# Optimization experiments

Measured on AMD Instinct MI355X. Metric: run time of the kernel, lower is better.

The kernel has to match this reference:

```python
import jax, jax.numpy as jnp
import numpy as np

B, T, E, H = 8, 2048, 256, 8
D = E // H  # head_size = 32
EPS = 1e-5  # torch LayerNorm default


def _layernorm(x, g, b):
    m = jnp.mean(x, axis=-1, keepdims=True)
    v = jnp.var(x, axis=-1, keepdims=True)
    return (x - m) / jnp.sqrt(v + EPS) * g + b


def setup_inputs() -> dict:
    key = jax.random.key(0)
    ks = jax.random.split(key, 9)
    s = lambda k, shape, fan: (jax.random.normal(k, shape, jnp.float32) / np.sqrt(fan)).astype(jnp.float32)
    return {
        "x": jax.random.normal(ks[0], (B, T, E), jnp.float32),
        "wq": s(ks[1], (H, E, D), E),
        "wk": s(ks[2], (H, E, D), E),
        "wv": s(ks[3], (H, E, D), E),
        "w_lin": s(ks[4], (E, E), E),
        "b_lin": jnp.zeros((E,), jnp.float32),
        "g1": jnp.ones((E,), jnp.float32),
        "beta1": jnp.zeros((E,), jnp.float32),
        "g2": jnp.ones((E,), jnp.float32),
        "beta2": jnp.zeros((E,), jnp.float32),
        "w_f1": s(ks[5], (E, 4 * E), E),
        "b_f1": jnp.zeros((4 * E,), jnp.float32),
        "w_f2": s(ks[6], (4 * E, E), 4 * E),
        "b_f2": jnp.zeros((E,), jnp.float32),
    }


def reference(x, wq, wk, wv, w_lin, b_lin, g1, beta1, g2, beta2, w_f1, b_f1, w_f2, b_f2):
    b, t, e = x.shape
    xn = _layernorm(x, g1, beta1)  # norm1
    # all heads at once: (B,T,E) x (H,E,D) -> (B,H,T,D)
    q = jnp.einsum('bte,hed->bhtd', xn, wq)
    k = jnp.einsum('bte,hed->bhtd', xn, wk)
    v = jnp.einsum('bte,hed->bhtd', xn, wv)
    # scale uses C = embedding_size (as in source, not head_size)
    scores = jnp.einsum('bhtd,bhsd->bhts', q, k) * (e ** -0.5)
    mask = jnp.tril(jnp.ones((t, t), bool))  # (query t, key s)
    scores = jnp.where(mask[None, None, :, :], scores, -jnp.inf)
    # source applies softmax over dim=1 of (B,T,T) = the QUERY axis -> axis 2 of bhts
    attn = jax.nn.softmax(scores, axis=2)
    heads = jnp.einsum('bhts,bhsd->bhtd', attn, v)
    heads = heads.transpose(0, 2, 1, 3).reshape(b, t, e)  # concat over heads
    xh = xn + heads  # residual around attention
    xl = xh @ w_lin + b_lin  # projection (dropout is identity at eval)
    x2 = _layernorm(xl, g2, beta2)  # norm2
    ff = jax.nn.relu(x2 @ w_f1 + b_f1) @ w_f2 + b_f2  # FFN (dropout identity)
    return x2 + ff
```

## Files before the change

### kernel.cpp

```cpp
#include <hip/hip_runtime.h>
#include <math.h>

#define TT 2048
#define TE 256
#define NTOK 16384
#define QSCALE (0.0625f * 1.44269504088896f)

typedef short  bf16x8 __attribute__((ext_vector_type(8)));
typedef float  f32x4  __attribute__((ext_vector_type(4)));
typedef float  f32x16 __attribute__((ext_vector_type(16)));
typedef unsigned short u16x4 __attribute__((ext_vector_type(4)));
typedef unsigned short u16x8 __attribute__((ext_vector_type(8)));

__device__ __forceinline__ unsigned short f2b(float f) {
    union { float f; unsigned int u; } v; v.f = f;
    unsigned int r = v.u + 0x7FFF + ((v.u >> 16) & 1);
    return (unsigned short)(r >> 16);
}
__device__ __forceinline__ float b2f(unsigned short u) {
    union { unsigned int i; float f; } v; v.i = ((unsigned int)u) << 16;
    return v.f;
}
#if __has_builtin(__builtin_amdgcn_cvt_pk_bf16_f32)
__device__ __forceinline__ unsigned int pk_bf16(float a, float b) {
    typedef __bf16 bf2 __attribute__((ext_vector_type(2)));
    union { bf2 v; unsigned int u; } u;
    u.v = __builtin_amdgcn_cvt_pk_bf16_f32(a, b);
    return u.u;
}
#else
__device__ __forceinline__ unsigned int pk_bf16(float a, float b) {
    return (unsigned int)f2b(a) | ((unsigned int)f2b(b) << 16);
}
#endif
#if __has_builtin(__builtin_amdgcn_exp2f)
#define FEXP2(x) __builtin_amdgcn_exp2f(x)
#else
#define FEXP2(x) __expf(0.69314718056f * (x))
#endif
__device__ __forceinline__ void pswap(unsigned &a, unsigned &b) {
#if __has_builtin(__builtin_amdgcn_permlane32_swap)
    auto r = __builtin_amdgcn_permlane32_swap(a, b, false, false);
    a = r[0]; b = r[1];
#else
    asm("v_permlane32_swap_b32 %0, %1" : "+v"(a), "+v"(b));
#endif
}
__device__ __forceinline__ bf16x8 ld8(const unsigned short* p) {
    return *(const bf16x8*)p;
}
__device__ __forceinline__ void gl_lds16(const unsigned short* g, unsigned short* l) {
    __builtin_amdgcn_global_load_lds(
        (const __attribute__((address_space(1))) unsigned int*)(uintptr_t)g,
        (__attribute__((address_space(3))) unsigned int*)(uintptr_t)l,
        16, 0, 0);
}
#define MFMA16(a, b, c) __builtin_amdgcn_mfma_f32_16x16x32_bf16((a), (b), (c), 0, 0, 0)
#define MFMA32(a, b, c) __builtin_amdgcn_mfma_f32_32x32x16_bf16((a), (b), (c), 0, 0, 0)
#define SETPRIO(n) __builtin_amdgcn_s_setprio(n)


__device__ __forceinline__ void soft_pv(const f32x16 st, bf16x8 vv0, bf16x8 vv1,
                                        bool diag, int hi, int l31, f32x16& acc) {
    unsigned Wd[8];
    if (diag) {
#pragma unroll
        for (int j = 0; j < 8; ++j) {
            int r0 = 2 * j;
            int s0 = (r0 & 3) + 8 * (r0 >> 2) + 4 * hi;
            float e0 = (s0 <= l31)     ? FEXP2(st[r0])     : 0.f;
            float e1 = (s0 + 1 <= l31) ? FEXP2(st[r0 + 1]) : 0.f;
            Wd[j] = pk_bf16(e0, e1);
        }
    } else {
#pragma unroll
        for (int j = 0; j < 8; ++j)
            Wd[j] = pk_bf16(FEXP2(st[2 * j]), FEXP2(st[2 * j + 1]));
    }
    pswap(Wd[0], Wd[2]); pswap(Wd[1], Wd[3]);
    pswap(Wd[4], Wd[6]); pswap(Wd[5], Wd[7]);
    union { unsigned u4[4]; bf16x8 v; } pa0, pa1;
    pa0.u4[0] = Wd[0]; pa0.u4[1] = Wd[1]; pa0.u4[2] = Wd[2]; pa0.u4[3] = Wd[3];
    pa1.u4[0] = Wd[4]; pa1.u4[1] = Wd[5]; pa1.u4[2] = Wd[6]; pa1.u4[3] = Wd[7];
    SETPRIO(1);
    acc = MFMA32(pa0.v, vv0, acc);
    acc = MFMA32(pa1.v, vv1, acc);
    SETPRIO(0);
}

__device__ __forceinline__ void accum_exp(const f32x16 st, bool diag,
                                          int hi, int l31, float* acc) {
    if (diag) {
#pragma unroll
        for (int r = 0; r < 16; ++r) {
            int s_local = (r & 3) + 8 * (r >> 2) + 4 * hi;
            acc[r] += (l31 >= s_local) ? FEXP2(st[r]) : 0.f;
        }
    } else {
#pragma unroll
        for (int r = 0; r < 16; ++r) acc[r] += FEXP2(st[r]);
    }
}

__global__ __launch_bounds__(256) void prep(const float* __restrict__ wq,
                                            const float* __restrict__ wk,
                                            const float* __restrict__ wv,
                                            const float* __restrict__ w_lin,
                                            const float* __restrict__ w_f1,
                                            const float* __restrict__ w_f2,
                                            unsigned short* __restrict__ Wqkv,
                                            unsigned short* __restrict__ Wlin,
                                            unsigned short* __restrict__ Wf1,
                                            unsigned short* __restrict__ Wf2,
                                            const float* __restrict__ X,
                                            const float* __restrict__ g,
                                            const float* __restrict__ bta,
                                            unsigned short* __restrict__ Yb) {
    if (blockIdx.x >= 3072) {
        int row = (blockIdx.x - 3072) * 4 + (threadIdx.x >> 6);
        int lane = threadIdx.x & 63;
        const float4 v = *(const float4*)&X[(size_t)row * TE + lane * 4];
        float s = v.x + v.y + v.z + v.w;
        float s2 = v.x * v.x + v.y * v.y + v.z * v.z + v.w * v.w;
#pragma unroll
        for (int off = 1; off <= 32; off <<= 1) {
            s  += __shfl_xor(s,  off, 64);
            s2 += __shfl_xor(s2, off, 64);
        }
        float mean = s * (1.0f / TE);
        float var = s2 * (1.0f / TE) - mean * mean;
        float rstd = rsqrtf(var + 1e-5f);
        const float4 gg = *(const float4*)&g[lane * 4];
        const float4 bb = *(const float4*)&bta[lane * 4];
        u16x4 ob = { f2b((v.x - mean) * rstd * gg.x + bb.x),
                     f2b((v.y - mean) * rstd * gg.y + bb.y),
                     f2b((v.z - mean) * rstd * gg.z + bb.z),
                     f2b((v.w - mean) * rstd * gg.w + bb.w) };
        *(u16x4*)&Yb[(size_t)row * TE + lane * 4] = ob;
        return;
    }
    int idx = blockIdx.x * 256 + threadIdx.x;
    if (idx < 196608) {
        int n = idx >> 8, k = idx & 255;
        int which = n >> 8, h = (n >> 5) & 7, d = n & 31;
        const float* w = (which == 0) ? wq : (which == 1) ? wk : wv;
        Wqkv[idx] = f2b(w[(h * 256 + k) * 32 + d]);
    } else if (idx < 262144) {
        int i = idx - 196608; int n = i >> 8, k = i & 255;
        Wlin[i] = f2b(w_lin[k * 256 + n]);
    } else if (idx < 524288) {
        int i = idx - 262144; int n = i >> 8, k = i & 255;
        Wf1[i] = f2b(w_f1[k * 1024 + n]);
    } else {
        int i = idx - 524288; int n = i >> 10, k = i & 1023;
        Wf2[i] = f2b(w_f2[k * 256 + n]);
    }
}

__global__ __launch_bounds__(256) void ln2_red(const float* __restrict__ Pp,
                                               const float* __restrict__ bias,
                                               const float* __restrict__ g,
                                               const float* __restrict__ bta,
                                               unsigned short* __restrict__ Yb) {
    int row = blockIdx.x * 4 + (threadIdx.x >> 6);
    int lane = threadIdx.x & 63;
    size_t base = (size_t)row * TE + lane * 4;
    const float4 p0 = *(const float4*)&Pp[base];
    const float4 bl = *(const float4*)&bias[lane * 4];
    float4 v;
    v.x = p0.x + bl.x; v.y = p0.y + bl.y;
    v.z = p0.z + bl.z; v.w = p0.w + bl.w;
    float s = v.x + v.y + v.z + v.w;
    float s2 = v.x * v.x + v.y * v.y + v.z * v.z + v.w * v.w;
#pragma unroll
    for (int off = 1; off <= 32; off <<= 1) {
        s  += __shfl_xor(s,  off, 64);
        s2 += __shfl_xor(s2, off, 64);
    }
    float mean = s * (1.0f / TE);
    float var = s2 * (1.0f / TE) - mean * mean;
    float rstd = rsqrtf(var + 1e-5f);
    const float4 gg = *(const float4*)&g[lane * 4];
    const float4 bb = *(const float4*)&bta[lane * 4];
    u16x4 ob = { f2b((v.x - mean) * rstd * gg.x + bb.x),
                 f2b((v.y - mean) * rstd * gg.y + bb.y),
                 f2b((v.z - mean) * rstd * gg.z + bb.z),
                 f2b((v.w - mean) * rstd * gg.w + bb.w) };
    *(u16x4*)&Yb[base] = ob;
}

template<int KS>
__global__ __launch_bounds__(256) void gemm_lds(const unsigned short* __restrict__ A,
                                                int lda,
                                                const unsigned short* __restrict__ Bt,
                                                int ldb,
                                                const float* __restrict__ bias,
                                                const unsigned short* __restrict__ resid,
                                                float* __restrict__ outF,
                                                unsigned short* __restrict__ outB,
                                                int N, int relu) {
    __shared__ unsigned short LDSb[3 * 2048 + 3 * 4096];
    unsigned short* Al = LDSb;
    unsigned short* Bl = LDSb + 3 * 2048;
    int tid = threadIdx.x;
    int w = tid >> 6, lane = tid & 63, q = lane >> 4, col = lane & 15;
    int wm = w & 1, wn = w >> 1;
    int m0 = blockIdx.x * 64;
    int n0 = blockIdx.y * 128;
    f32x4 acc[2][4] = {};
    int srow = lane >> 2;
    int skq  = ((lane & 3) ^ ((srow >> 1) & 3)) * 8;
    const unsigned short* Ag0 = A  + (size_t)(m0 + w * 16 + srow) * lda + skq;
    const unsigned short* Bg0 = Bt + (size_t)(n0 + w * 32 + srow) * ldb + skq;
    const unsigned short* Bg1 = Bg0 + (size_t)16 * ldb;
    int rq = (q ^ ((col >> 1) & 3)) * 8;
#define G_STAGE(bf, kk) do { \
        gl_lds16(Ag0 + (kk), &Al[(bf) * 2048 + (w * 16) * 32]); \
        gl_lds16(Bg0 + (kk), &Bl[(bf) * 4096 + (w * 32) * 32]); \
        gl_lds16(Bg1 + (kk), &Bl[(bf) * 4096 + (w * 32 + 16) * 32]); \
    } while (0)
    G_STAGE(0, 0);
    G_STAGE(1, 32);
#pragma unroll
    for (int k0 = 0; k0 < KS; k0 += 32) {
        const int jb = (k0 >> 5) % 3;
        if (k0 + 32 < KS) { asm volatile("s_waitcnt vmcnt(3)" ::: "memory"); }
        else              { asm volatile("s_waitcnt vmcnt(0)" ::: "memory"); }
        __builtin_amdgcn_s_barrier();
        if (k0 + 64 < KS) G_STAGE((jb + 2) % 3, k0 + 64);
        bf16x8 a[2], b[4];
#pragma unroll
        for (int i = 0; i < 2; ++i)
            a[i] = ld8(&Al[jb * 2048 + (wm * 32 + i * 16 + col) * 32 + rq]);
#pragma unroll
        for (int j = 0; j < 4; ++j)
            b[j] = ld8(&Bl[jb * 4096 + (wn * 64 + j * 16 + col) * 32 + rq]);
#pragma unroll
        for (int i = 0; i < 2; ++i)
#pragma unroll
            for (int j = 0; j < 4; ++j)
                acc[i][j] = MFMA16(a[i], b[j], acc[i][j]);
        __builtin_amdgcn_sched_barrier(0);
    }
#undef G_STAGE
    float* Cb = (float*)LDSb;
    const int CLD = 132;
#pragma unroll
    for (int i = 0; i < 2; ++i) {
        __syncthreads();
#pragma unroll
        for (int j = 0; j < 4; ++j)
#pragma unroll
            for (int r = 0; r < 4; ++r)
                Cb[(wm * 16 + q * 4 + r) * CLD + wn * 64 + j * 16 + col] = acc[i][j][r];
        __syncthreads();
        int row = tid >> 3;
        int seg = (tid & 7) * 16;
        int mloc = (row & 15) + i * 16 + (row >> 4) * 32;
        int m = m0 + mloc;
        int n = n0 + seg;
        float vbuf[16];
#pragma unroll
        for (int u = 0; u < 16; ++u) vbuf[u] = Cb[row * CLD + seg + u];
        if (bias) {
#pragma unroll
            for (int u4 = 0; u4 < 4; ++u4) {
                float4 bb = *(const float4*)&bias[n + u4 * 4];
                vbuf[u4 * 4 + 0] += bb.x; vbuf[u4 * 4 + 1] += bb.y;
                vbuf[u4 * 4 + 2] += bb.z; vbuf[u4 * 4 + 3] += bb.w;
            }
        }
        if (resid) {
            u16x8 r0 = *(const u16x8*)&resid[(size_t)m * N + n];
            u16x8 r1 = *(const u16x8*)&resid[(size_t)m * N + n + 8];
#pragma unroll
            for (int u = 0; u < 8; ++u) {
                vbuf[u]     += b2f(r0[u]);
                vbuf[8 + u] += b2f(r1[u]);
            }
        }
        if (relu) {
#pragma unroll
            for (int u = 0; u < 16; ++u) vbuf[u] = fmaxf(vbuf[u], 0.f);
        }
        if (outF) {
#pragma unroll
            for (int u = 0; u < 16; u += 4)
                *(float4*)&outF[(size_t)m * N + n + u] = *(const float4*)&vbuf[u];
        }
        if (outB) {
            u16x8 o0, o1;
#pragma unroll
            for (int u = 0; u < 8; ++u) { o0[u] = f2b(vbuf[u]); o1[u] = f2b(vbuf[8 + u]); }
            *(u16x8*)&outB[(size_t)m * N + n] = o0;
            *(u16x8*)&outB[(size_t)m * N + n + 8] = o1;
        }
    }
}

__global__ __launch_bounds__(256) void gemm_qkv(const unsigned short* __restrict__ A,
                                                const unsigned short* __restrict__ Bt,
                                                unsigned short* __restrict__ Qd,
                                                unsigned short* __restrict__ Kd,
                                                unsigned short* __restrict__ Vc) {
    const int K = 256;
    __shared__ unsigned short LDSb[3 * 2048 + 3 * 4096];
    unsigned short* Al = LDSb;
    unsigned short* Bl = LDSb + 3 * 2048;
    int tid = threadIdx.x;
    int w = tid >> 6, lane = tid & 63, q = lane >> 4, col = lane & 15;
    int wm = w & 1, wn = w >> 1;
    int m0 = blockIdx.x * 64;
    int n0 = blockIdx.y * 128;
    f32x4 acc[2][4] = {};
    int srow = lane >> 2;
    int skq  = ((lane & 3) ^ ((srow >> 1) & 3)) * 8;
    const unsigned short* Ag0 = A  + (size_t)(m0 + w * 16 + srow) * K + skq;
    const unsigned short* Bg0 = Bt + (size_t)(n0 + w * 32 + srow) * K + skq;
    const unsigned short* Bg1 = Bg0 + (size_t)16 * K;
    int rq = (q ^ ((col >> 1) & 3)) * 8;
#define G_STAGE(bf, kk) do { \
        gl_lds16(Ag0 + (kk), &Al[(bf) * 2048 + (w * 16) * 32]); \
        gl_lds16(Bg0 + (kk), &Bl[(bf) * 4096 + (w * 32) * 32]); \
        gl_lds16(Bg1 + (kk), &Bl[(bf) * 4096 + (w * 32 + 16) * 32]); \
    } while (0)
    G_STAGE(0, 0);
    G_STAGE(1, 32);
#pragma unroll
    for (int k0 = 0; k0 < K; k0 += 32) {
        const int jb = (k0 >> 5) % 3;
        if (k0 + 32 < K) { asm volatile("s_waitcnt vmcnt(3)" ::: "memory"); }
        else             { asm volatile("s_waitcnt vmcnt(0)" ::: "memory"); }
        __builtin_amdgcn_s_barrier();
        if (k0 + 64 < K) G_STAGE((jb + 2) % 3, k0 + 64);
        bf16x8 a[2], b[4];
#pragma unroll
        for (int i = 0; i < 2; ++i)
            a[i] = ld8(&Al[jb * 2048 + (wm * 32 + i * 16 + col) * 32 + rq]);
#pragma unroll
        for (int j = 0; j < 4; ++j)
            b[j] = ld8(&Bl[jb * 4096 + (wn * 64 + j * 16 + col) * 32 + rq]);
#pragma unroll
        for (int i = 0; i < 2; ++i)
#pragma unroll
            for (int j = 0; j < 4; ++j)
                acc[i][j] = MFMA16(a[i], b[j], acc[i][j]);
        __builtin_amdgcn_sched_barrier(0);
    }
#undef G_STAGE
#pragma unroll
    for (int i = 0; i < 2; ++i)
#pragma unroll
    for (int j = 0; j < 4; ++j) {
        int n = n0 + wn * 64 + j * 16 + col;
        int which = n >> 8, h = (n >> 5) & 7, d = n & 31;
        int m = m0 + wm * 32 + i * 16 + q * 4;
        int b = m >> 11, t = m & 2047;
        int bh = b * 8 + h;
        if (which == 0) {
            size_t qb = ((size_t)(bh * 2 + (d >> 4)) * TT + t) * 16 + (d & 15);
#pragma unroll
            for (int r = 0; r < 4; ++r)
                Qd[qb + r * 16] = f2b(acc[i][j][r] * QSCALE);
        } else if (which == 1) {
            size_t kb = ((size_t)(bh * 2 + (d >> 4)) * TT + t) * 16 + (d & 15);
#pragma unroll
            for (int r = 0; r < 4; ++r)
                Kd[kb + r * 16] = f2b(acc[i][j][r]);
        } else {
            uint2 pv;
            pv.x = pk_bf16(acc[i][j][0], acc[i][j][1]);
            pv.y = pk_bf16(acc[i][j][2], acc[i][j][3]);
            *(uint2*)&Vc[(((size_t)bh * 256 + (t >> 3)) * 32 + d) * 8 + (t & 7)] = pv;
        }
    }
}

__global__ __launch_bounds__(256, 2) void attn_cols(const unsigned short* __restrict__ Qd,
                                                    const unsigned short* __restrict__ Kd,
                                                    unsigned short* __restrict__ Vc) {
    __shared__ float Lb[4][32];
    __shared__ float Linv[32];
    int tid = threadIdx.x;
    int w = tid >> 6, lane = tid & 63, hi = lane >> 5, l31 = lane & 31;
    int bh = blockIdx.x;
    int u = blockIdx.y;
    const unsigned short* Qb = Qd + ((size_t)bh * 2 * TT + l31) * 16 + hi * 8;
    const unsigned short* Kb = Kd + ((size_t)bh * 2 * TT + l31) * 16 + hi * 8;
    const f32x16 z16 = {};
#pragma unroll
    for (int phase = 0; phase < 2; ++phase) {
        int stile = phase ? (63 - u) : u;
        int sbase = stile * 32;
        bf16x8 a0 = ld8(Kb + (size_t)sbase * 16);
        bf16x8 a1 = ld8(Kb + ((size_t)TT + sbase) * 16);
        float acc[16] = {};
        int c = stile + w;
        bool diagP = (w == 0);
        bf16x8 qP0, qP1, qQ0, qQ1;
        if (c < 64) {
            qP0 = ld8(Qb + (size_t)(c * 32) * 16);
            qP1 = ld8(Qb + ((size_t)TT + c * 32) * 16);
        }
        if (c + 4 < 64) {
            qQ0 = ld8(Qb + (size_t)((c + 4) * 32) * 16);
            qQ1 = ld8(Qb + ((size_t)TT + (c + 4) * 32) * 16);
        }
        while (c + 8 < 64) {
            SETPRIO(1);
            f32x16 stP = MFMA32(a0, qP0, z16); stP = MFMA32(a1, qP1, stP);
            SETPRIO(0);
            qP0 = ld8(Qb + (size_t)((c + 8) * 32) * 16);
            qP1 = ld8(Qb + ((size_t)TT + (c + 8) * 32) * 16);
            SETPRIO(1);
            f32x16 stQ = MFMA32(a0, qQ0, z16); stQ = MFMA32(a1, qQ1, stQ);
            SETPRIO(0);
            accum_exp(stP, diagP, hi, l31, acc); diagP = false;
            if (c + 12 < 64) {
                qQ0 = ld8(Qb + (size_t)((c + 12) * 32) * 16);
                qQ1 = ld8(Qb + ((size_t)TT + (c + 12) * 32) * 16);
            }
            accum_exp(stQ, false, hi, l31, acc);
            c += 8;
        }
        if (c < 64) {
            f32x16 stP = MFMA32(a0, qP0, z16); stP = MFMA32(a1, qP1, stP);
            accum_exp(stP, diagP, hi, l31, acc);
        }
        if (c + 4 < 64) {
            f32x16 stQ = MFMA32(a0, qQ0, z16); stQ = MFMA32(a1, qQ1, stQ);
            accum_exp(stQ, false, hi, l31, acc);
        }
#pragma unroll
        for (int off = 1; off <= 16; off <<= 1)
#pragma unroll
            for (int r = 0; r < 16; ++r) acc[r] += __shfl_xor(acc[r], off, 64);
        if (l31 == 0) {
#pragma unroll
            for (int r = 0; r < 16; ++r) {
                int s_local = (r & 3) + 8 * (r >> 2) + 4 * hi;
                Lb[w][s_local] = acc[r];
            }
        }
        __syncthreads();
        if (tid < 32)
            Linv[tid] = 1.0f / (Lb[0][tid] + Lb[1][tid] + Lb[2][tid] + Lb[3][tid]);
        __syncthreads();
        if (tid < 128) {
            int sbl = tid >> 5;
            int d = tid & 31;
            size_t base = (((size_t)bh * 256 + stile * 4 + sbl) * 32 + d) * 8;
            u16x8 v = *(const u16x8*)&Vc[base];
            u16x8 o;
#pragma unroll
            for (int e = 0; e < 8; ++e) o[e] = f2b(b2f(v[e]) * Linv[sbl * 8 + e]);
            *(u16x8*)&Vc[base] = o;
        }
        __syncthreads();
    }
}

__global__ __launch_bounds__(256, 2) void attn_out(const unsigned short* __restrict__ Qd,
                                                   const unsigned short* __restrict__ Kd,
                                                   const unsigned short* __restrict__ Vc,
                                                   const unsigned short* __restrict__ xnb,
                                                   unsigned short* __restrict__ xh_bf) {
    __shared__ float Ob[4][16][36];
    int tid = threadIdx.x;
    int w = tid >> 6, lane = tid & 63, hi = lane >> 5, l31 = lane & 31;
    int bh = blockIdx.x, b = bh >> 3, h = bh & 7;
    int u = blockIdx.y;
    const unsigned short* Kb = Kd + ((size_t)bh * 2 * TT + l31) * 16 + hi * 8;
    const unsigned short* Vb = Vc + (size_t)bh * 65536 + hi * 256 + l31 * 8;
    const unsigned short* Qbase = Qd + ((size_t)bh * 2 * TT + l31) * 16 + hi * 8;
    const f32x16 z16 = {};

#pragma unroll
    for (int phase = 0; phase < 2; ++phase) {
        int tt = phase ? (63 - u) : u;
        int tbase = tt * 32;
        bf16x8 q0 = ld8(Qbase + (size_t)tbase * 16);
        bf16x8 q1 = ld8(Qbase + ((size_t)TT + tbase) * 16);
        f32x16 acc = z16;

        int c = w;
        bf16x8 kP0, kP1, vP0, vP1, kQ0, kQ1, vQ0, vQ1;
        if (c <= tt) {
            kP0 = ld8(Kb + (size_t)c * 512);
            kP1 = ld8(Kb + (size_t)TT * 16 + (size_t)c * 512);
            vP0 = ld8(Vb + (size_t)c * 1024);
            vP1 = ld8(Vb + (size_t)c * 1024 + 512);
        }
        if (c + 4 <= tt) {
            kQ0 = ld8(Kb + (size_t)(c + 4) * 512);
            kQ1 = ld8(Kb + (size_t)TT * 16 + (size_t)(c + 4) * 512);
            vQ0 = ld8(Vb + (size_t)(c + 4) * 1024);
            vQ1 = ld8(Vb + (size_t)(c + 4) * 1024 + 512);
        }
        while (c + 8 <= tt) {
            SETPRIO(1);
            f32x16 stP = MFMA32(kP0, q0, z16); stP = MFMA32(kP1, q1, stP);
            SETPRIO(0);
            kP0 = ld8(Kb + (size_t)(c + 8) * 512);
            kP1 = ld8(Kb + (size_t)TT * 16 + (size_t)(c + 8) * 512);
            SETPRIO(1);
            f32x16 stQ = MFMA32(kQ0, q0, z16); stQ = MFMA32(kQ1, q1, stQ);
            SETPRIO(0);
            soft_pv(stP, vP0, vP1, false, hi, l31, acc);
            vP0 = ld8(Vb + (size_t)(c + 8) * 1024);
            vP1 = ld8(Vb + (size_t)(c + 8) * 1024 + 512);
            if (c + 12 <= tt) {
                kQ0 = ld8(Kb + (size_t)(c + 12) * 512);
                kQ1 = ld8(Kb + (size_t)TT * 16 + (size_t)(c + 12) * 512);
            }
            soft_pv(stQ, vQ0, vQ1, false, hi, l31, acc);
            if (c + 12 <= tt) {
                vQ0 = ld8(Vb + (size_t)(c + 12) * 1024);
                vQ1 = ld8(Vb + (size_t)(c + 12) * 1024 + 512);
            }
            c += 8;
        }
        if (c <= tt) {
            f32x16 stP = MFMA32(kP0, q0, z16); stP = MFMA32(kP1, q1, stP);
            soft_pv(stP, vP0, vP1, c == tt, hi, l31, acc);
        }
        if (c + 4 <= tt) {
            f32x16 stQ = MFMA32(kQ0, q0, z16); stQ = MFMA32(kQ1, q1, stQ);
            soft_pv(stQ, vQ0, vQ1, c + 4 == tt, hi, l31, acc);
        }

#pragma unroll
        for (int half = 0; half < 2; ++half) {
#pragma unroll
            for (int rr = 0; rr < 8; ++rr) {
                int r = half * 8 + rr;
                int t16 = (r & 3) + 8 * ((r >> 2) & 1) + 4 * hi;
                Ob[w][t16][l31] = acc[r];
            }
            __syncthreads();
            if (tid < 128) {
                int row = tid >> 3;
                int c4 = (tid & 7) * 4;
                float4 s0 = *(const float4*)&Ob[0][row][c4];
                float4 s1 = *(const float4*)&Ob[1][row][c4];
                float4 s2 = *(const float4*)&Ob[2][row][c4];
                float4 s3 = *(const float4*)&Ob[3][row][c4];
                size_t base = ((size_t)(b * TT) + tbase + half * 16 + row) * TE
                              + h * 32 + c4;
                u16x4 xv = *(const u16x4*)&xnb[base];
                u16x4 ob = { f2b(s0.x + s1.x + s2.x + s3.x + b2f(xv[0])),
                             f2b(s0.y + s1.y + s2.y + s3.y + b2f(xv[1])),
                             f2b(s0.z + s1.z + s2.z + s3.z + b2f(xv[2])),
                             f2b(s0.w + s1.w + s2.w + s3.w + b2f(xv[3])) };
                *(u16x4*)&xh_bf[base] = ob;
            }
            __syncthreads();
        }
    }
}

extern "C" void kernel_launch(void* const* d_in, const int* in_sizes, int n_in,
                              void* d_out, int out_size, void* d_ws, size_t ws_size,
                              hipStream_t stream) {
    (void)in_sizes; (void)n_in; (void)out_size; (void)ws_size;
    const float* x     = (const float*)d_in[0];
    const float* wq    = (const float*)d_in[1];
    const float* wk    = (const float*)d_in[2];
    const float* wv    = (const float*)d_in[3];
    const float* w_lin = (const float*)d_in[4];
    const float* b_lin = (const float*)d_in[5];
    const float* g1    = (const float*)d_in[6];
    const float* beta1 = (const float*)d_in[7];
    const float* g2    = (const float*)d_in[8];
    const float* beta2 = (const float*)d_in[9];
    const float* w_f1  = (const float*)d_in[10];
    const float* b_f1  = (const float*)d_in[11];
    const float* w_f2  = (const float*)d_in[12];
    const float* b_f2  = (const float*)d_in[13];
    float* out = (float*)d_out;

    char* ws = (char*)d_ws;
    unsigned short* Wqkv_t = (unsigned short*)(ws + 0);
    unsigned short* Wlin_t = (unsigned short*)(ws + 393216);
    unsigned short* Wf1_t  = (unsigned short*)(ws + 524288);
    unsigned short* Wf2_t  = (unsigned short*)(ws + 1048576);
    unsigned short* xn_bf  = (unsigned short*)(ws + 2097152);
    unsigned short* Qbf    = (unsigned short*)(ws + 10485760);
    unsigned short* Kbf    = (unsigned short*)(ws + 18874368);
    unsigned short* Vt     = (unsigned short*)(ws + 27262976);
    unsigned short* xh_bf  = (unsigned short*)(ws + 35651584);
    float*          Pp     = (float*)(ws + 44040192);
    unsigned short* x2_bf  = xn_bf;
    unsigned short* h_bf   = Qbf;

    prep<<<7168, 256, 0, stream>>>(wq, wk, wv, w_lin, w_f1, w_f2,
                                   Wqkv_t, Wlin_t, Wf1_t, Wf2_t,
                                   x, g1, beta1, xn_bf);
    gemm_qkv<<<dim3(256, 6), 256, 0, stream>>>(xn_bf, Wqkv_t, Qbf, Kbf, Vt);
    attn_cols<<<dim3(64, 32), 256, 0, stream>>>(Qbf, Kbf, Vt);
    attn_out<<<dim3(64, 32), 256, 0, stream>>>(Qbf, Kbf, Vt, xn_bf, xh_bf);
    gemm_lds<256><<<dim3(256, 2), 256, 0, stream>>>(xh_bf, 256, Wlin_t, 256,
                                                    nullptr, nullptr, Pp, nullptr, 256, 0);
    ln2_red<<<4096, 256, 0, stream>>>(Pp, b_lin, g2, beta2, x2_bf);
    gemm_lds<256><<<dim3(256, 8), 256, 0, stream>>>(x2_bf, 256, Wf1_t, 256,
                                                    b_f1, nullptr, nullptr, h_bf, 1024, 1);
    gemm_lds<1024><<<dim3(256, 2), 256, 0, stream>>>(h_bf, 1024, Wf2_t, 1024,
                                                     b_f2, x2_bf, out, nullptr, 256, 0);
}
```

Baseline: 225.8 us.

## Tile weight transposes through LDS and split attention blocks to one tile each

The weight-prep path now transposes weights with 64x64 tiles staged in shared memory, so global reads and writes are coalesced. Before, each thread did one strided scalar gather, and the prep grid shrinks accordingly. Both attention kernels drop the paired-tile (u, 63-u) load-balancing loop and launch one block per tile, doubling the grid. This raises parallelism but makes per-block work uneven under the causal mask.

```diff
diff --git a/kernel.cpp b/kernel.cpp
--- a/kernel.cpp
+++ b/kernel.cpp
@@ -116,8 +116,9 @@
                                             const float* __restrict__ g,
                                             const float* __restrict__ bta,
                                             unsigned short* __restrict__ Yb) {
-    if (blockIdx.x >= 3072) {
-        int row = (blockIdx.x - 3072) * 4 + (threadIdx.x >> 6);
+    int bid = blockIdx.x;
+    if (bid >= 240) {
+        int row = (bid - 240) * 4 + (threadIdx.x >> 6);
         int lane = threadIdx.x & 63;
         const float4 v = *(const float4*)&X[(size_t)row * TE + lane * 4];
         float s = v.x + v.y + v.z + v.w;
@@ -139,21 +140,43 @@
         *(u16x4*)&Yb[(size_t)row * TE + lane * 4] = ob;
         return;
     }
-    int idx = blockIdx.x * 256 + threadIdx.x;
-    if (idx < 196608) {
-        int n = idx >> 8, k = idx & 255;
-        int which = n >> 8, h = (n >> 5) & 7, d = n & 31;
-        const float* w = (which == 0) ? wq : (which == 1) ? wk : wv;
-        Wqkv[idx] = f2b(w[(h * 256 + k) * 32 + d]);
-    } else if (idx < 262144) {
-        int i = idx - 196608; int n = i >> 8, k = i & 255;
-        Wlin[i] = f2b(w_lin[k * 256 + n]);
-    } else if (idx < 524288) {
-        int i = idx - 262144; int n = i >> 8, k = i & 255;
-        Wf1[i] = f2b(w_f1[k * 1024 + n]);
-    } else {
-        int i = idx - 524288; int n = i >> 10, k = i & 1023;
-        Wf2[i] = f2b(w_f2[k * 256 + n]);
+    __shared__ unsigned short Tt[64][65];
+    int t = threadIdx.x;
+    if (bid < 96) {
+        int which = bid / 32, h = (bid >> 2) & 7, kt = bid & 3;
+        const float* src = ((which == 0) ? wq : (which == 1) ? wk : wv)
+                           + (size_t)h * 256 * 32;
+        int d = t & 31, kr = t >> 5;
+#pragma unroll
+        for (int r = 0; r < 8; ++r) {
+            int kl = kr * 8 + r;
+            Tt[kl][d] = f2b(src[(size_t)(kt * 64 + kl) * 32 + d]);
+        }
+        __syncthreads();
+        int kl = t & 63, dr = t >> 6;
+#pragma unroll
+        for (int r = 0; r < 8; ++r) {
+            int dl = dr * 8 + r;
+            Wqkv[(size_t)(which * 256 + h * 32 + dl) * 256 + kt * 64 + kl] = Tt[kl][dl];
+        }
+        return;
+    }
+    const float* src; unsigned short* dst; int ldn, ldk, kt, nt;
+    if (bid < 112)      { int b2 = bid - 96;  src = w_lin; dst = Wlin; ldn = 256;  ldk = 256;  kt = b2 & 3;  nt = b2 >> 2; }
+    else if (bid < 176) { int b3 = bid - 112; src = w_f1;  dst = Wf1;  ldn = 1024; ldk = 256;  kt = b3 >> 4; nt = b3 & 15; }
+    else                { int b4 = bid - 176; src = w_f2;  dst = Wf2;  ldn = 256;  ldk = 1024; kt = b4 >> 2; nt = b4 & 3; }
+    int n = t & 63, kr = t >> 6;
+#pragma unroll
+    for (int r = 0; r < 16; ++r) {
+        int kl = kr * 16 + r;
+        Tt[kl][n] = f2b(src[(size_t)(kt * 64 + kl) * ldn + nt * 64 + n]);
+    }
+    __syncthreads();
+    int klane = t & 63, nr = t >> 6;
+#pragma unroll
+    for (int r = 0; r < 16; ++r) {
+        int nl = nr * 16 + r;
+        dst[(size_t)(nt * 64 + nl) * ldk + kt * 64 + klane] = Tt[klane][nl];
     }
 }
 
@@ -384,79 +407,74 @@
     int tid = threadIdx.x;
     int w = tid >> 6, lane = tid & 63, hi = lane >> 5, l31 = lane & 31;
     int bh = blockIdx.x;
-    int u = blockIdx.y;
+    int stile = blockIdx.y;
     const unsigned short* Qb = Qd + ((size_t)bh * 2 * TT + l31) * 16 + hi * 8;
     const unsigned short* Kb = Kd + ((size_t)bh * 2 * TT + l31) * 16 + hi * 8;
     const f32x16 z16 = {};
-#pragma unroll
-    for (int phase = 0; phase < 2; ++phase) {
-        int stile = phase ? (63 - u) : u;
-        int sbase = stile * 32;
-        bf16x8 a0 = ld8(Kb + (size_t)sbase * 16);
-        bf16x8 a1 = ld8(Kb + ((size_t)TT + sbase) * 16);
-        float acc[16] = {};
-        int c = stile + w;
-        bool diagP = (w == 0);
-        bf16x8 qP0, qP1, qQ0, qQ1;
-        if (c < 64) {
-            qP0 = ld8(Qb + (size_t)(c * 32) * 16);
-            qP1 = ld8(Qb + ((size_t)TT + c * 32) * 16);
-        }
-        if (c + 4 < 64) {
-            qQ0 = ld8(Qb + (size_t)((c + 4) * 32) * 16);
-            qQ1 = ld8(Qb + ((size_t)TT + (c + 4) * 32) * 16);
-        }
-        while (c + 8 < 64) {
-            SETPRIO(1);
-            f32x16 stP = MFMA32(a0, qP0, z16); stP = MFMA32(a1, qP1, stP);
-            SETPRIO(0);
-            qP0 = ld8(Qb + (size_t)((c + 8) * 32) * 16);
-            qP1 = ld8(Qb + ((size_t)TT + (c + 8) * 32) * 16);
-            SETPRIO(1);
-            f32x16 stQ = MFMA32(a0, qQ0, z16); stQ = MFMA32(a1, qQ1, stQ);
-            SETPRIO(0);
-            accum_exp(stP, diagP, hi, l31, acc); diagP = false;
-            if (c + 12 < 64) {
-                qQ0 = ld8(Qb + (size_t)((c + 12) * 32) * 16);
-                qQ1 = ld8(Qb + ((size_t)TT + (c + 12) * 32) * 16);
-            }
-            accum_exp(stQ, false, hi, l31, acc);
-            c += 8;
-        }
-        if (c < 64) {
-            f32x16 stP = MFMA32(a0, qP0, z16); stP = MFMA32(a1, qP1, stP);
-            accum_exp(stP, diagP, hi, l31, acc);
-        }
-        if (c + 4 < 64) {
-            f32x16 stQ = MFMA32(a0, qQ0, z16); stQ = MFMA32(a1, qQ1, stQ);
-            accum_exp(stQ, false, hi, l31, acc);
-        }
-#pragma unroll
-        for (int off = 1; off <= 16; off <<= 1)
-#pragma unroll
-            for (int r = 0; r < 16; ++r) acc[r] += __shfl_xor(acc[r], off, 64);
-        if (l31 == 0) {
-#pragma unroll
-            for (int r = 0; r < 16; ++r) {
-                int s_local = (r & 3) + 8 * (r >> 2) + 4 * hi;
-                Lb[w][s_local] = acc[r];
-            }
-        }
-        __syncthreads();
-        if (tid < 32)
-            Linv[tid] = 1.0f / (Lb[0][tid] + Lb[1][tid] + Lb[2][tid] + Lb[3][tid]);
-        __syncthreads();
-        if (tid < 128) {
-            int sbl = tid >> 5;
-            int d = tid & 31;
-            size_t base = (((size_t)bh * 256 + stile * 4 + sbl) * 32 + d) * 8;
-            u16x8 v = *(const u16x8*)&Vc[base];
-            u16x8 o;
-#pragma unroll
-            for (int e = 0; e < 8; ++e) o[e] = f2b(b2f(v[e]) * Linv[sbl * 8 + e]);
-            *(u16x8*)&Vc[base] = o;
-        }
-        __syncthreads();
+    int sbase = stile * 32;
+    bf16x8 a0 = ld8(Kb + (size_t)sbase * 16);
+    bf16x8 a1 = ld8(Kb + ((size_t)TT + sbase) * 16);
+    float acc[16] = {};
+    int c = stile + w;
+    bool diagP = (w == 0);
+    bf16x8 qP0, qP1, qQ0, qQ1;
+    if (c < 64) {
+        qP0 = ld8(Qb + (size_t)(c * 32) * 16);
+        qP1 = ld8(Qb + ((size_t)TT + c * 32) * 16);
+    }
+    if (c + 4 < 64) {
+        qQ0 = ld8(Qb + (size_t)((c + 4) * 32) * 16);
+        qQ1 = ld8(Qb + ((size_t)TT + (c + 4) * 32) * 16);
+    }
+    while (c + 8 < 64) {
+        SETPRIO(1);
+        f32x16 stP = MFMA32(a0, qP0, z16); stP = MFMA32(a1, qP1, stP);
+        SETPRIO(0);
+        qP0 = ld8(Qb + (size_t)((c + 8) * 32) * 16);
+        qP1 = ld8(Qb + ((size_t)TT + (c + 8) * 32) * 16);
+        SETPRIO(1);
+        f32x16 stQ = MFMA32(a0, qQ0, z16); stQ = MFMA32(a1, qQ1, stQ);
+        SETPRIO(0);
+        accum_exp(stP, diagP, hi, l31, acc); diagP = false;
+        if (c + 12 < 64) {
+            qQ0 = ld8(Qb + (size_t)((c + 12) * 32) * 16);
+            qQ1 = ld8(Qb + ((size_t)TT + (c + 12) * 32) * 16);
+        }
+        accum_exp(stQ, false, hi, l31, acc);
+        c += 8;
+    }
+    if (c < 64) {
+        f32x16 stP = MFMA32(a0, qP0, z16); stP = MFMA32(a1, qP1, stP);
+        accum_exp(stP, diagP, hi, l31, acc);
+    }
+    if (c + 4 < 64) {
+        f32x16 stQ = MFMA32(a0, qQ0, z16); stQ = MFMA32(a1, qQ1, stQ);
+        accum_exp(stQ, false, hi, l31, acc);
+    }
+#pragma unroll
+    for (int off = 1; off <= 16; off <<= 1)
+#pragma unroll
+        for (int r = 0; r < 16; ++r) acc[r] += __shfl_xor(acc[r], off, 64);
+    if (l31 == 0) {
+#pragma unroll
+        for (int r = 0; r < 16; ++r) {
+            int s_local = (r & 3) + 8 * (r >> 2) + 4 * hi;
+            Lb[w][s_local] = acc[r];
+        }
+    }
+    __syncthreads();
+    if (tid < 32)
+        Linv[tid] = 1.0f / (Lb[0][tid] + Lb[1][tid] + Lb[2][tid] + Lb[3][tid]);
+    __syncthreads();
+    if (tid < 128) {
+        int sbl = tid >> 5;
+        int d = tid & 31;
+        size_t base = (((size_t)bh * 256 + stile * 4 + sbl) * 32 + d) * 8;
+        u16x8 v = *(const u16x8*)&Vc[base];
+        u16x8 o;
+#pragma unroll
+        for (int e = 0; e < 8; ++e) o[e] = f2b(b2f(v[e]) * Linv[sbl * 8 + e]);
+        *(u16x8*)&Vc[base] = o;
     }
 }
 
@@ -469,93 +487,89 @@
     int tid = threadIdx.x;
     int w = tid >> 6, lane = tid & 63, hi = lane >> 5, l31 = lane & 31;
     int bh = blockIdx.x, b = bh >> 3, h = bh & 7;
-    int u = blockIdx.y;
+    int tt = blockIdx.y;
     const unsigned short* Kb = Kd + ((size_t)bh * 2 * TT + l31) * 16 + hi * 8;
     const unsigned short* Vb = Vc + (size_t)bh * 65536 + hi * 256 + l31 * 8;
     const unsigned short* Qbase = Qd + ((size_t)bh * 2 * TT + l31) * 16 + hi * 8;
     const f32x16 z16 = {};
 
-#pragma unroll
-    for (int phase = 0; phase < 2; ++phase) {
-        int tt = phase ? (63 - u) : u;
-        int tbase = tt * 32;
-        bf16x8 q0 = ld8(Qbase + (size_t)tbase * 16);
-        bf16x8 q1 = ld8(Qbase + ((size_t)TT + tbase) * 16);
-        f32x16 acc = z16;
-
-        int c = w;
-        bf16x8 kP0, kP1, vP0, vP1, kQ0, kQ1, vQ0, vQ1;
-        if (c <= tt) {
-            kP0 = ld8(Kb + (size_t)c * 512);
-            kP1 = ld8(Kb + (size_t)TT * 16 + (size_t)c * 512);
-            vP0 = ld8(Vb + (size_t)c * 1024);
-            vP1 = ld8(Vb + (size_t)c * 1024 + 512);
-        }
-        if (c + 4 <= tt) {
-            kQ0 = ld8(Kb + (size_t)(c + 4) * 512);
-            kQ1 = ld8(Kb + (size_t)TT * 16 + (size_t)(c + 4) * 512);
-            vQ0 = ld8(Vb + (size_t)(c + 4) * 1024);
-            vQ1 = ld8(Vb + (size_t)(c + 4) * 1024 + 512);
-        }
-        while (c + 8 <= tt) {
-            SETPRIO(1);
-            f32x16 stP = MFMA32(kP0, q0, z16); stP = MFMA32(kP1, q1, stP);
-            SETPRIO(0);
-            kP0 = ld8(Kb + (size_t)(c + 8) * 512);
-            kP1 = ld8(Kb + (size_t)TT * 16 + (size_t)(c + 8) * 512);
-            SETPRIO(1);
-            f32x16 stQ = MFMA32(kQ0, q0, z16); stQ = MFMA32(kQ1, q1, stQ);
-            SETPRIO(0);
-            soft_pv(stP, vP0, vP1, false, hi, l31, acc);
-            vP0 = ld8(Vb + (size_t)(c + 8) * 1024);
-            vP1 = ld8(Vb + (size_t)(c + 8) * 1024 + 512);
-            if (c + 12 <= tt) {
-                kQ0 = ld8(Kb + (size_t)(c + 12) * 512);
-                kQ1 = ld8(Kb + (size_t)TT * 16 + (size_t)(c + 12) * 512);
-            }
-            soft_pv(stQ, vQ0, vQ1, false, hi, l31, acc);
-            if (c + 12 <= tt) {
-                vQ0 = ld8(Vb + (size_t)(c + 12) * 1024);
-                vQ1 = ld8(Vb + (size_t)(c + 12) * 1024 + 512);
-            }
-            c += 8;
-        }
-        if (c <= tt) {
-            f32x16 stP = MFMA32(kP0, q0, z16); stP = MFMA32(kP1, q1, stP);
-            soft_pv(stP, vP0, vP1, c == tt, hi, l31, acc);
-        }
-        if (c + 4 <= tt) {
-            f32x16 stQ = MFMA32(kQ0, q0, z16); stQ = MFMA32(kQ1, q1, stQ);
-            soft_pv(stQ, vQ0, vQ1, c + 4 == tt, hi, l31, acc);
-        }
-
-#pragma unroll
-        for (int half = 0; half < 2; ++half) {
-#pragma unroll
-            for (int rr = 0; rr < 8; ++rr) {
-                int r = half * 8 + rr;
-                int t16 = (r & 3) + 8 * ((r >> 2) & 1) + 4 * hi;
-                Ob[w][t16][l31] = acc[r];
-            }
-            __syncthreads();
-            if (tid < 128) {
-                int row = tid >> 3;
-                int c4 = (tid & 7) * 4;
-                float4 s0 = *(const float4*)&Ob[0][row][c4];
-                float4 s1 = *(const float4*)&Ob[1][row][c4];
-                float4 s2 = *(const float4*)&Ob[2][row][c4];
-                float4 s3 = *(const float4*)&Ob[3][row][c4];
-                size_t base = ((size_t)(b * TT) + tbase + half * 16 + row) * TE
-                              + h * 32 + c4;
-                u16x4 xv = *(const u16x4*)&xnb[base];
-                u16x4 ob = { f2b(s0.x + s1.x + s2.x + s3.x + b2f(xv[0])),
-                             f2b(s0.y + s1.y + s2.y + s3.y + b2f(xv[1])),
-                             f2b(s0.z + s1.z + s2.z + s3.z + b2f(xv[2])),
-                             f2b(s0.w + s1.w + s2.w + s3.w + b2f(xv[3])) };
-                *(u16x4*)&xh_bf[base] = ob;
-            }
-            __syncthreads();
-        }
+    int tbase = tt * 32;
+    bf16x8 q0 = ld8(Qbase + (size_t)tbase * 16);
+    bf16x8 q1 = ld8(Qbase + ((size_t)TT + tbase) * 16);
+    f32x16 acc = z16;
+
+    int c = w;
+    bf16x8 kP0, kP1, vP0, vP1, kQ0, kQ1, vQ0, vQ1;
+    if (c <= tt) {
+        kP0 = ld8(Kb + (size_t)c * 512);
+        kP1 = ld8(Kb + (size_t)TT * 16 + (size_t)c * 512);
+        vP0 = ld8(Vb + (size_t)c * 1024);
+        vP1 = ld8(Vb + (size_t)c * 1024 + 512);
+    }
+    if (c + 4 <= tt) {
+        kQ0 = ld8(Kb + (size_t)(c + 4) * 512);
+        kQ1 = ld8(Kb + (size_t)TT * 16 + (size_t)(c + 4) * 512);
+        vQ0 = ld8(Vb + (size_t)(c + 4) * 1024);
+        vQ1 = ld8(Vb + (size_t)(c + 4) * 1024 + 512);
+    }
+    while (c + 8 <= tt) {
+        SETPRIO(1);
+        f32x16 stP = MFMA32(kP0, q0, z16); stP = MFMA32(kP1, q1, stP);
+        SETPRIO(0);
+        kP0 = ld8(Kb + (size_t)(c + 8) * 512);
+        kP1 = ld8(Kb + (size_t)TT * 16 + (size_t)(c + 8) * 512);
+        SETPRIO(1);
+        f32x16 stQ = MFMA32(kQ0, q0, z16); stQ = MFMA32(kQ1, q1, stQ);
+        SETPRIO(0);
+        soft_pv(stP, vP0, vP1, false, hi, l31, acc);
+        vP0 = ld8(Vb + (size_t)(c + 8) * 1024);
+        vP1 = ld8(Vb + (size_t)(c + 8) * 1024 + 512);
+        if (c + 12 <= tt) {
+            kQ0 = ld8(Kb + (size_t)(c + 12) * 512);
+            kQ1 = ld8(Kb + (size_t)TT * 16 + (size_t)(c + 12) * 512);
+        }
+        soft_pv(stQ, vQ0, vQ1, false, hi, l31, acc);
+        if (c + 12 <= tt) {
+            vQ0 = ld8(Vb + (size_t)(c + 12) * 1024);
+            vQ1 = ld8(Vb + (size_t)(c + 12) * 1024 + 512);
+        }
+        c += 8;
+    }
+    if (c <= tt) {
+        f32x16 stP = MFMA32(kP0, q0, z16); stP = MFMA32(kP1, q1, stP);
+        soft_pv(stP, vP0, vP1, c == tt, hi, l31, acc);
+    }
+    if (c + 4 <= tt) {
+        f32x16 stQ = MFMA32(kQ0, q0, z16); stQ = MFMA32(kQ1, q1, stQ);
+        soft_pv(stQ, vQ0, vQ1, c + 4 == tt, hi, l31, acc);
+    }
+
+#pragma unroll
+    for (int half = 0; half < 2; ++half) {
+#pragma unroll
+        for (int rr = 0; rr < 8; ++rr) {
+            int r = half * 8 + rr;
+            int t16 = (r & 3) + 8 * ((r >> 2) & 1) + 4 * hi;
+            Ob[w][t16][l31] = acc[r];
+        }
+        __syncthreads();
+        if (tid < 128) {
+            int row = tid >> 3;
+            int c4 = (tid & 7) * 4;
+            float4 s0 = *(const float4*)&Ob[0][row][c4];
+            float4 s1 = *(const float4*)&Ob[1][row][c4];
+            float4 s2 = *(const float4*)&Ob[2][row][c4];
+            float4 s3 = *(const float4*)&Ob[3][row][c4];
+            size_t base = ((size_t)(b * TT) + tbase + half * 16 + row) * TE
+                          + h * 32 + c4;
+            u16x4 xv = *(const u16x4*)&xnb[base];
+            u16x4 ob = { f2b(s0.x + s1.x + s2.x + s3.x + b2f(xv[0])),
+                         f2b(s0.y + s1.y + s2.y + s3.y + b2f(xv[1])),
+                         f2b(s0.z + s1.z + s2.z + s3.z + b2f(xv[2])),
+                         f2b(s0.w + s1.w + s2.w + s3.w + b2f(xv[3])) };
+            *(u16x4*)&xh_bf[base] = ob;
+        }
+        __syncthreads();
     }
 }
 
@@ -593,12 +607,12 @@
     unsigned short* x2_bf  = xn_bf;
     unsigned short* h_bf   = Qbf;
 
-    prep<<<7168, 256, 0, stream>>>(wq, wk, wv, w_lin, w_f1, w_f2,
+    prep<<<4336, 256, 0, stream>>>(wq, wk, wv, w_lin, w_f1, w_f2,
                                    Wqkv_t, Wlin_t, Wf1_t, Wf2_t,
                                    x, g1, beta1, xn_bf);
     gemm_qkv<<<dim3(256, 6), 256, 0, stream>>>(xn_bf, Wqkv_t, Qbf, Kbf, Vt);
-    attn_cols<<<dim3(64, 32), 256, 0, stream>>>(Qbf, Kbf, Vt);
-    attn_out<<<dim3(64, 32), 256, 0, stream>>>(Qbf, Kbf, Vt, xn_bf, xh_bf);
+    attn_cols<<<dim3(64, 64), 256, 0, stream>>>(Qbf, Kbf, Vt);
+    attn_out<<<dim3(64, 64), 256, 0, stream>>>(Qbf, Kbf, Vt, xn_bf, xh_bf);
     gemm_lds<256><<<dim3(256, 2), 256, 0, stream>>>(xh_bf, 256, Wlin_t, 256,
                                                     nullptr, nullptr, Pp, nullptr, 256, 0);
     ln2_red<<<4096, 256, 0, stream>>>(Pp, b_lin, g2, beta2, x2_bf);
```

Result: no change. 222.4 us (-1.5%).
